# Kernel tuning notes

Hardware: AMD Instinct MI355X
Metric: run time of the kernel (lower is better)

The kernel has to match this reference:

```python
import jax, jax.numpy as jnp
import numpy as np

B, S, D = 2, 2048, 1024
H, KV, HD = 16, 4, 64
E, TOPK, F = 8, 2, 2048
EPS = 1e-5
THETA = 10000.0


def setup_inputs() -> dict:
    key = jax.random.key(0)
    ks = jax.random.split(key, 12)
    sc = 0.02
    x = jax.random.normal(ks[0], (B, S, D), jnp.float32)
    # real RoPE tables
    inv = 1.0 / (THETA ** (np.arange(0, HD, 2, dtype=np.float32) / HD))
    t = np.arange(S, dtype=np.float32)
    f = np.outer(t, inv)  # [S, HD/2]
    freqs_cos = jnp.asarray(np.cos(f), jnp.float32)
    freqs_sin = jnp.asarray(np.sin(f), jnp.float32)
    return {
        "x": x,
        "freqs_cos": freqs_cos,
        "freqs_sin": freqs_sin,
        "attn_norm_w": jnp.ones((D,), jnp.float32),
        "ffn_norm_w": jnp.ones((D,), jnp.float32),
        "wq": jax.random.normal(ks[1], (D, H * HD), jnp.float32) * sc,
        "wk": jax.random.normal(ks[2], (D, KV * HD), jnp.float32) * sc,
        "wv": jax.random.normal(ks[3], (D, KV * HD), jnp.float32) * sc,
        "wo": jax.random.normal(ks[4], (H * HD, D), jnp.float32) * sc,
        "gate_w": jax.random.normal(ks[5], (D, E), jnp.float32) * sc,
        "w1": jax.random.normal(ks[6], (E, D, F), jnp.float32) * sc,
        "w2": jax.random.normal(ks[7], (E, F, D), jnp.float32) * sc,
        "w3": jax.random.normal(ks[8], (E, D, F), jnp.float32) * sc,
    }


def rmsnorm(x, w):
    return x * jax.lax.rsqrt(jnp.mean(x * x, axis=-1, keepdims=True) + EPS) * w


def apply_rope(xq, cos, sin):
    # xq: [B,S,h,HD]; cos/sin: [S, HD/2]
    xr, xi = xq[..., 0::2], xq[..., 1::2]
    c = cos[None, :, None, :]
    s = sin[None, :, None, :]
    out = jnp.stack([xr * c - xi * s, xr * s + xi * c], axis=-1)
    return out.reshape(xq.shape)


def attention(xn, freqs_cos, freqs_sin, wq, wk, wv, wo):
    q = (xn @ wq).reshape(B, S, H, HD)
    k = (xn @ wk).reshape(B, S, KV, HD)
    v = (xn @ wv).reshape(B, S, KV, HD)
    q = apply_rope(q, freqs_cos, freqs_sin)
    k = apply_rope(k, freqs_cos, freqs_sin)
    n_rep = H // KV
    k = jnp.repeat(k, n_rep, axis=2)  # [B,S,H,HD]
    v = jnp.repeat(v, n_rep, axis=2)
    scores = jnp.einsum("bqhd,bkhd->bhqk", q, k) / jnp.sqrt(jnp.float32(HD))
    causal = jnp.tril(jnp.ones((S, S), bool))
    scores = jnp.where(causal[None, None], scores, jnp.finfo(scores.dtype).min)
    probs = jax.nn.softmax(scores, axis=-1)
    out = jnp.einsum("bhqk,bkhd->bqhd", probs, v).reshape(B, S, H * HD)
    return out @ wo


def sparse_moe(hn, gate_w, w1, w2, w3):
    xf = hn.reshape(-1, D)  # [T, D]
    probs = jax.nn.softmax(xf @ gate_w, axis=-1)  # [T, E]
    topv, topi = jax.lax.top_k(probs, TOPK)
    topv = topv / jnp.sum(topv, axis=-1, keepdims=True)
    # dense [T, E] routing weights (0 for non-selected experts)
    wdense = jnp.sum(jax.nn.one_hot(topi, E, dtype=xf.dtype) * topv[..., None], axis=1)
    h1 = jax.nn.silu(jnp.einsum("td,edf->etf", xf, w1))
    h3 = jnp.einsum("td,edf->etf", xf, w3)
    y = jnp.einsum("etf,efd->etd", h1 * h3, w2)
    out = jnp.einsum("te,etd->td", wdense, y)
    return out.reshape(B, S, D)


def reference(x, freqs_cos, freqs_sin, attn_norm_w, ffn_norm_w,
              wq, wk, wv, wo, gate_w, w1, w2, w3):
    h = x + attention(rmsnorm(x, attn_norm_w), freqs_cos, freqs_sin, wq, wk, wv, wo)
    out = h + sparse_moe(rmsnorm(h, ffn_norm_w), gate_w, w1, w2, w3)
    return out
```

## Files before the change

### kernel.cpp

```cpp
#include <hip/hip_runtime.h>
#include <stdint.h>

typedef unsigned short u16;
typedef unsigned int u32;
typedef __attribute__((ext_vector_type(8))) short short8;
typedef __attribute__((ext_vector_type(8))) u16 us8;
typedef __attribute__((ext_vector_type(4))) u16 us4;
typedef __attribute__((ext_vector_type(4))) float f32x4;

constexpr int NB = 2;
constexpr int SEQ = 2048;
constexpr int DIM = 1024;
constexpr int NH = 16;
constexpr int HD = 64;
constexpr int NE = 8;
constexpr int FF = 2048;
constexpr int TOK = NB * SEQ;
constexpr int NQKV = 1536;
constexpr int NPAIR = TOK * 2;
constexpr float REPS = 1e-5f;

#define VMCNT(n) asm volatile("s_waitcnt vmcnt(" #n ")" ::: "memory")
#define LGKM0 asm volatile("s_waitcnt lgkmcnt(0)" ::: "memory")

__device__ __forceinline__ u16 f2bf(float x) {
  union { float f; u32 u; } v; v.f = x;
  u32 r = v.u + 0x7fffu + ((v.u >> 16) & 1u);
  return (u16)(r >> 16);
}
__device__ __forceinline__ float bf2f(u16 h) {
  union { u32 u; float f; } v; v.u = ((u32)h) << 16;
  return v.f;
}

__device__ __forceinline__ void gl_lds16(const u16* g, u16* l) {
  __builtin_amdgcn_global_load_lds(
      (const __attribute__((address_space(1))) void*)g,
      (__attribute__((address_space(3))) void*)l, 16, 0, 0);
}

template <bool SPLIT>
__global__ __launch_bounds__(256) void tcvt_k(const float* __restrict__ src,
                                              u16* __restrict__ dhi,
                                              u16* __restrict__ dlo,
                                              int K, int N) {
  int z = blockIdx.z;
  src += (size_t)z * K * N;
  dhi += (size_t)z * K * N;
  if (SPLIT) dlo += (size_t)z * K * N;
  int n0 = blockIdx.x * 64, k0 = blockIdx.y * 64;
  __shared__ float tile[64][65];
  int t = threadIdx.x;
  int kk = t >> 4, nn4 = (t & 15) * 4;
#pragma unroll
  for (int i = 0; i < 4; i++) {
    int k = kk + i * 16;
    const float* p = src + (size_t)(k0 + k) * N + n0 + nn4;
    float4 v = *(const float4*)p;
    tile[nn4 + 0][k] = v.x;
    tile[nn4 + 1][k] = v.y;
    tile[nn4 + 2][k] = v.z;
    tile[nn4 + 3][k] = v.w;
  }
  __syncthreads();
  int nn = t >> 4, k4 = (t & 15) * 4;
#pragma unroll
  for (int i = 0; i < 4; i++) {
    int n = nn + i * 16;
    us4 hi, lo;
#pragma unroll
    for (int j = 0; j < 4; j++) {
      float f = tile[n][k4 + j];
      u16 h = f2bf(f);
      hi[j] = h;
      if (SPLIT) lo[j] = f2bf(f - bf2f(h));
    }
    *(us4*)(dhi + (size_t)(n0 + n) * K + k0 + k4) = hi;
    if (SPLIT) *(us4*)(dlo + (size_t)(n0 + n) * K + k0 + k4) = lo;
  }
}

template <bool SPLIT>
__global__ __launch_bounds__(256) void rmsnorm_k(const float* __restrict__ x,
                                                 const float* __restrict__ w,
                                                 u16* __restrict__ ohi,
                                                 u16* __restrict__ olo) {
  int row = blockIdx.x, t = threadIdx.x;
  float4 v = *(const float4*)(x + (size_t)row * DIM + t * 4);
  float ss = v.x * v.x + v.y * v.y + v.z * v.z + v.w * v.w;
#pragma unroll
  for (int m = 1; m < 64; m <<= 1) ss += __shfl_xor(ss, m);
  __shared__ float red[4];
  if ((t & 63) == 0) red[t >> 6] = ss;
  __syncthreads();
  float rstd = rsqrtf((red[0] + red[1] + red[2] + red[3]) * (1.0f / DIM) + REPS);
  float4 wv = *(const float4*)(w + t * 4);
  float os[4] = {v.x * rstd * wv.x, v.y * rstd * wv.y, v.z * rstd * wv.z,
                 v.w * rstd * wv.w};
  us4 hi, lo;
#pragma unroll
  for (int j = 0; j < 4; j++) {
    u16 h = f2bf(os[j]);
    hi[j] = h;
    if (SPLIT) lo[j] = f2bf(os[j] - bf2f(h));
  }
  *(us4*)(ohi + (size_t)row * DIM + t * 4) = hi;
  if (SPLIT) *(us4*)(olo + (size_t)row * DIM + t * 4) = lo;
}

template <int EPI, bool SPLIT, bool DUAL, bool PERSIST, int NXL, int NT, int BN>
__global__ __launch_bounds__(256, 2) void gemm_k(
    const u16* __restrict__ Ah, const u16* __restrict__ Al,
    const u16* __restrict__ Bh, const u16* __restrict__ Bl,
    const u16* __restrict__ B1, int N, int ldc,
    float* __restrict__ Cf, u16* __restrict__ Cb, float* __restrict__ C2,
    const float* __restrict__ resid, const int* __restrict__ cnt,
    const int* __restrict__ pids, const float* __restrict__ pw,
    const int* __restrict__ plan) {
  constexpr int K = NT * 32;
  constexpr int WCOL = BN / 2;
  constexpr int FN = WCOL / 16;
  constexpr int NAI = 2;
  constexpr int NBI = BN / 64;
  constexpr int BUFA = 128 * 32;
  constexpr int BUFB = BN * 32;
  constexpr bool L6 = SPLIT || DUAL;

  int tid = threadIdx.x, lane = tid & 63, wid = tid >> 6;
  int wm = wid >> 1, wn = wid & 1;
  int rr = lane & 15, g = lane >> 4;

  __shared__ u16 sAh[3 * BUFA];
  __shared__ u16 sAl[SPLIT ? 3 * BUFA : 16];
  __shared__ u16 sBh[3 * BUFB];
  __shared__ u16 sBl[SPLIT ? 3 * BUFB : 16];
  __shared__ u16 sB1[DUAL ? 3 * BUFB : 16];
  __shared__ int spid[PERSIST ? 128 : 8];
  __shared__ int srow[PERSIST ? 128 : 8];

  int pl[9];
  int items;
  if (PERSIST) {
#pragma unroll
    for (int e = 0; e < 9; e++) pl[e] = plan[e];
    items = pl[8] << NXL;
  } else {
    items = 1;
  }

  int it0 = PERSIST ? blockIdx.x : 0;
  int itstep = PERSIST ? gridDim.x : 1;
  for (int w = it0; w < items; w += itstep) {
    int m0, n0, z, cntz;
    if (PERSIST) {
      int wy = w >> NXL;
      int x = w & ((1 << NXL) - 1);
      z = 0;
#pragma unroll
      for (int e = 1; e < 8; e++) z += (wy >= pl[e]) ? 1 : 0;
      int yt = wy - pl[z];
      m0 = yt * 128;
      n0 = x * BN;
      cntz = cnt[z];
      if (tid < 128) {
        int i = m0 + tid;
        if (i > cntz - 1) i = cntz - 1;
        int p = pids[z * NPAIR + i];
        spid[tid] = p;
        srow[tid] = (EPI == 2) ? (p >> 1) : p;
      }
      __syncthreads();
    } else {
      m0 = blockIdx.y * 128;
      n0 = blockIdx.x * BN;
      z = 0;
      cntz = 1 << 30;
    }

    const u16* Bhz = Bh + (size_t)z * N * K;
    const u16* Blz = SPLIT ? Bl + (size_t)z * N * K : nullptr;
    const u16* B1z = DUAL ? B1 + (size_t)z * N * K : nullptr;

    int p4 = lane & 3;
    const u16 *agh[NAI], *agl[NAI];
    int aoff[NAI];
#pragma unroll
    for (int i = 0; i < NAI; i++) {
      int rl = i * 64 + wid * 16 + (lane >> 2);
      int gr = PERSIST ? srow[rl] : (m0 + rl);
      int sc = p4 ^ ((rl >> 1) & 3);
      agh[i] = Ah + (size_t)gr * K + sc * 8;
      if (SPLIT) agl[i] = Al + (size_t)gr * K + sc * 8;
      aoff[i] = (i * 4 + wid) * 512;
    }
    const u16 *bgh[NBI], *bgl[NBI], *bg1[NBI];
    int boff[NBI];
#pragma unroll
    for (int i = 0; i < NBI; i++) {
      int rl = i * 64 + wid * 16 + (lane >> 2);
      int sc = p4 ^ ((rl >> 1) & 3);
      size_t gr = (size_t)(n0 + rl) * K + sc * 8;
      bgh[i] = Bhz + gr;
      if (SPLIT) bgl[i] = Blz + gr;
      if (DUAL) bg1[i] = B1z + gr;
      boff[i] = (i * 4 + wid) * 512;
    }

    auto STAGE = [&](int kt, int bi) {
      int k0 = kt * 32;
#pragma unroll
      for (int i = 0; i < NAI; i++) {
        gl_lds16(agh[i] + k0, sAh + bi * BUFA + aoff[i]);
        if (SPLIT) gl_lds16(agl[i] + k0, sAl + bi * BUFA + aoff[i]);
      }
#pragma unroll
      for (int i = 0; i < NBI; i++) {
        gl_lds16(bgh[i] + k0, sBh + bi * BUFB + boff[i]);
        if (SPLIT) gl_lds16(bgl[i] + k0, sBl + bi * BUFB + boff[i]);
        if (DUAL) gl_lds16(bg1[i] + k0, sB1 + bi * BUFB + boff[i]);
      }
    };

    f32x4 zv = {0.f, 0.f, 0.f, 0.f};
    f32x4 acc[4][FN];
    f32x4 acc1[DUAL ? 4 : 1][DUAL ? FN : 1];
#pragma unroll
    for (int a = 0; a < 4; a++)
#pragma unroll
      for (int b = 0; b < FN; b++) {
        acc[a][b] = zv;
        if (DUAL) acc1[a][b] = zv;
      }

    STAGE(0, 0);
    STAGE(1, 1);
    STAGE(2, 2);

    int bi = 0;
    for (int t = 0; t < NT; t++) {
      int og = NT - 1 - t;
      if (L6) {
        if (og >= 2) VMCNT(12);
        else if (og == 1) VMCNT(6);
        else VMCNT(0);
      } else {
        if (og >= 2) VMCNT(8);
        else if (og == 1) VMCNT(4);
        else VMCNT(0);
      }
      __builtin_amdgcn_s_barrier();

      const u16* bA = sAh + bi * BUFA;
      const u16* bAl = sAl + (SPLIT ? bi * BUFA : 0);
      const u16* bB = sBh + bi * BUFB;
      const u16* bBl = sBl + (SPLIT ? bi * BUFB : 0);
      const u16* bB1 = sB1 + (DUAL ? bi * BUFB : 0);

      short8 a_h[4], a_l[4], b_h[FN], b_l[FN], b1f[FN];
#pragma unroll
      for (int f = 0; f < 4; f++) {
        int ra = wm * 64 + f * 16 + rr;
        int off = ra * 32 + ((g ^ ((ra >> 1) & 3)) * 8);
        a_h[f] = *(const short8*)&bA[off];
        if (SPLIT) a_l[f] = *(const short8*)&bAl[off];
      }
#pragma unroll
      for (int f = 0; f < FN; f++) {
        int rb = wn * WCOL + f * 16 + rr;
        int off = rb * 32 + ((g ^ ((rb >> 1) & 3)) * 8);
        b_h[f] = *(const short8*)&bB[off];
        if (SPLIT) b_l[f] = *(const short8*)&bBl[off];
        if (DUAL) b1f[f] = *(const short8*)&bB1[off];
      }
#pragma unroll
      for (int fm = 0; fm < 4; fm++)
#pragma unroll
        for (int fn = 0; fn < FN; fn++) {
          acc[fm][fn] = __builtin_amdgcn_mfma_f32_16x16x32_bf16(
              a_h[fm], b_h[fn], acc[fm][fn], 0, 0, 0);
          if (SPLIT) {
            acc[fm][fn] = __builtin_amdgcn_mfma_f32_16x16x32_bf16(
                a_h[fm], b_l[fn], acc[fm][fn], 0, 0, 0);
            acc[fm][fn] = __builtin_amdgcn_mfma_f32_16x16x32_bf16(
                a_l[fm], b_h[fn], acc[fm][fn], 0, 0, 0);
          }
          if (DUAL)
            acc1[fm][fn] = __builtin_amdgcn_mfma_f32_16x16x32_bf16(
                a_h[fm], b1f[fn], acc1[fm][fn], 0, 0, 0);
        }

      LGKM0;
      __builtin_amdgcn_s_barrier();
      if (t + 3 < NT) STAGE(t + 3, bi);
      bi = (bi == 2) ? 0 : bi + 1;
    }

#pragma unroll
    for (int fm = 0; fm < 4; fm++)
#pragma unroll
      for (int fn = 0; fn < FN; fn++)
#pragma unroll
        for (int rg = 0; rg < 4; rg++) {
          int rl = wm * 64 + fm * 16 + g * 4 + rg;
          int col = n0 + wn * WCOL + fn * 16 + rr;
          float v = acc[fm][fn][rg];
          if (EPI == 0) {
            Cf[(size_t)(m0 + rl) * ldc + col] = v;
          } else if (EPI == 1) {
            size_t idx = (size_t)(m0 + rl) * ldc + col;
            float r2 = v + resid[idx];
            Cf[idx] = r2;
            C2[idx] = r2;
          } else if (EPI == 2) {
            if (m0 + rl < cntz) {
              float gg = v / (1.0f + __expf(-v));
              float o = gg * acc1[fm][fn][rg];
              Cb[(size_t)spid[rl] * ldc + col] = f2bf(o);
            }
          } else {
            if (m0 + rl < cntz) {
              int p = spid[rl];
              atomicAdd(&Cf[(size_t)(p >> 1) * ldc + col], pw[p] * v);
            }
          }
        }
    if (PERSIST) __syncthreads();
  }
}

__global__ __launch_bounds__(256) void rope_k(float* __restrict__ qkv,
                                              const float* __restrict__ fc,
                                              const float* __restrict__ fs) {
  int idx = blockIdx.x * 256 + threadIdx.x;
  int i = idx & 31;
  int hh = (idx >> 5) % 20;
  int t = idx / 640;
  if (t >= TOK) return;
  int s = t & (SEQ - 1);
  int base = (hh < 16) ? (hh * 64) : (1024 + (hh - 16) * 64);
  float c = fc[s * 32 + i], sn = fs[s * 32 + i];
  float* p = qkv + (size_t)t * NQKV + base + 2 * i;
  float xr = p[0], xi = p[1];
  p[0] = xr * c - xi * sn;
  p[1] = xr * sn + xi * c;
}

__global__ __launch_bounds__(256) void cvtkv_k(const float* __restrict__ qkv,
                                               u16* __restrict__ Kh,
                                               u16* __restrict__ Kl,
                                               u16* __restrict__ Vh,
                                               u16* __restrict__ Vl) {
  int kvt = blockIdx.x;
  int kvh = blockIdx.y;
  int b = blockIdx.z;
  int t = threadIdx.x;
  __shared__ float vt[64][65];
  size_t tile = ((size_t)((b * 4 + kvh) * 32 + kvt)) * 4096;
  int r = t >> 2, c4 = t & 3;
  {
    const float* kp = qkv + ((size_t)(b * SEQ + kvt * 64 + r)) * NQKV + 1024 +
                      kvh * 64 + c4 * 16;
    float ff[16];
#pragma unroll
    for (int q = 0; q < 4; q++) {
      float4 f = *(const float4*)(kp + q * 4);
      ff[q * 4 + 0] = f.x; ff[q * 4 + 1] = f.y;
      ff[q * 4 + 2] = f.z; ff[q * 4 + 3] = f.w;
    }
#pragma unroll
    for (int half = 0; half < 2; half++) {
      int c = c4 * 2 + half;
      us8 hi, lo;
#pragma unroll
      for (int j = 0; j < 8; j++) {
        float f = ff[half * 8 + j];
        u16 h = f2bf(f);
        hi[j] = h;
        lo[j] = f2bf(f - bf2f(h));
      }
      int off = r * 64 + ((c ^ (r & 7)) * 8);
      *(us8*)(Kh + tile + off) = hi;
      *(us8*)(Kl + tile + off) = lo;
    }
  }
  {
    const float* vp = qkv + ((size_t)(b * SEQ + kvt * 64 + r)) * NQKV + 1280 +
                      kvh * 64 + c4 * 16;
#pragma unroll
    for (int q = 0; q < 4; q++) {
      float4 f = *(const float4*)(vp + q * 4);
      vt[r][c4 * 16 + q * 4 + 0] = f.x;
      vt[r][c4 * 16 + q * 4 + 1] = f.y;
      vt[r][c4 * 16 + q * 4 + 2] = f.z;
      vt[r][c4 * 16 + q * 4 + 3] = f.w;
    }
  }
  __syncthreads();
  {
    int d = t >> 2, g4 = t & 3;
    float ff[16];
#pragma unroll
    for (int j = 0; j < 16; j++) ff[j] = vt[g4 * 16 + j][d];
#pragma unroll
    for (int half = 0; half < 2; half++) {
      int c = g4 * 2 + half;
      us8 hi, lo;
#pragma unroll
      for (int j = 0; j < 8; j++) {
        float f = ff[half * 8 + j];
        u16 h = f2bf(f);
        hi[j] = h;
        lo[j] = f2bf(f - bf2f(h));
      }
      int off = d * 64 + ((c ^ (d & 7)) * 8);
      *(us8*)(Vh + tile + off) = hi;
      *(us8*)(Vl + tile + off) = lo;
    }
  }
}

__global__ __launch_bounds__(256, 2) void flash_k(
    const float* __restrict__ qkv, const u16* __restrict__ Kg,
    const u16* __restrict__ Klg, const u16* __restrict__ Vg,
    const u16* __restrict__ Vlg, u16* __restrict__ ah, u16* __restrict__ al) {
  int pi = blockIdx.x;
  int h = blockIdx.y;
  int b = blockIdx.z;
  int qt[2] = {31 - pi, pi};
  int kvh = h >> 2;
  int tid = threadIdx.x, lane = tid & 63, wid = tid >> 6;
  int rr = lane & 15, g = lane >> 4;

  __shared__ u16 sKh[4096], sKl[4096], sVh[4096], sVl[4096];
  __shared__ u32 sP[4][1024];

  f32x4 zv = {0.f, 0.f, 0.f, 0.f};
  short8 aqh[2][2], aql[2][2];
#pragma unroll
  for (int u = 0; u < 2; u++) {
    int qrow = qt[u] * 64 + wid * 16 + rr;
    const float* qp =
        qkv + ((size_t)(b * SEQ + qrow)) * NQKV + h * 64 + g * 8;
#pragma unroll
    for (int kc = 0; kc < 2; kc++) {
      float4 f0 = *(const float4*)(qp + kc * 32);
      float4 f1 = *(const float4*)(qp + kc * 32 + 4);
      float ff[8] = {f0.x, f0.y, f0.z, f0.w, f1.x, f1.y, f1.z, f1.w};
#pragma unroll
      for (int j = 0; j < 8; j++) {
        u16 hi = f2bf(ff[j]);
        aqh[u][kc][j] = (short)hi;
        aql[u][kc][j] = (short)f2bf(ff[j] - bf2f(hi));
      }
    }
  }

  f32x4 o[2][4];
  float m_r[2][4], l_r[2][4];
#pragma unroll
  for (int u = 0; u < 2; u++)
#pragma unroll
    for (int i = 0; i < 4; i++) {
      o[u][i] = zv;
      m_r[u][i] = -3.0e38f;
      l_r[u][i] = 0.f;
    }

  size_t tb = ((size_t)(b * 4 + kvh) * 32) * 4096;
  int so = tid * 16;
  us8 rKh[2], rKl[2], rVh[2], rVl[2];
  {
    size_t go = tb + so;
    rKh[0] = *(const us8*)(Kg + go);  rKh[1] = *(const us8*)(Kg + go + 8);
    rKl[0] = *(const us8*)(Klg + go); rKl[1] = *(const us8*)(Klg + go + 8);
    rVh[0] = *(const us8*)(Vg + go);  rVh[1] = *(const us8*)(Vg + go + 8);
    rVl[0] = *(const us8*)(Vlg + go); rVl[1] = *(const us8*)(Vlg + go + 8);
  }

  int nt = qt[0];
  for (int kvt = 0; kvt <= nt; kvt++) {
    __syncthreads();
    *(us8*)&sKh[so] = rKh[0]; *(us8*)&sKh[so + 8] = rKh[1];
    *(us8*)&sKl[so] = rKl[0]; *(us8*)&sKl[so + 8] = rKl[1];
    *(us8*)&sVh[so] = rVh[0]; *(us8*)&sVh[so + 8] = rVh[1];
    *(us8*)&sVl[so] = rVl[0]; *(us8*)&sVl[so + 8] = rVl[1];
    if (kvt < nt) {
      size_t go = tb + (size_t)(kvt + 1) * 4096 + so;
      rKh[0] = *(const us8*)(Kg + go);  rKh[1] = *(const us8*)(Kg + go + 8);
      rKl[0] = *(const us8*)(Klg + go); rKl[1] = *(const us8*)(Klg + go + 8);
      rVh[0] = *(const us8*)(Vg + go);  rVh[1] = *(const us8*)(Vg + go + 8);
      rVl[0] = *(const us8*)(Vlg + go); rVl[1] = *(const us8*)(Vlg + go + 8);
    }
    __syncthreads();

#pragma unroll
    for (int u = 0; u < 2; u++) {
      if (!(u == 1 && kvt > qt[1])) {
        float pv[4][4];
#pragma unroll
        for (int c16 = 0; c16 < 4; c16++) {
          int rk = c16 * 16 + rr;
          f32x4 sacc = zv;
#pragma unroll
          for (int kc = 0; kc < 2; kc++) {
            int sw = rk * 64 + (((kc * 4 + g) ^ (rk & 7)) * 8);
            short8 bh = *(const short8*)&sKh[sw];
            short8 bl = *(const short8*)&sKl[sw];
            sacc = __builtin_amdgcn_mfma_f32_16x16x32_bf16(aqh[u][kc], bh,
                                                           sacc, 0, 0, 0);
            sacc = __builtin_amdgcn_mfma_f32_16x16x32_bf16(aqh[u][kc], bl,
                                                           sacc, 0, 0, 0);
            sacc = __builtin_amdgcn_mfma_f32_16x16x32_bf16(aql[u][kc], bh,
                                                           sacc, 0, 0, 0);
          }
          bool diag = (kvt == qt[u]);
#pragma unroll
          for (int rg = 0; rg < 4; rg++) {
            float val = sacc[rg] * 0.125f;
            if (diag) {
              int kv_l = c16 * 16 + rr;
              int q_l = wid * 16 + g * 4 + rg;
              if (kv_l > q_l) val = -3.0e38f;
            }
            pv[c16][rg] = val;
          }
        }
        float pm[4];
#pragma unroll
        for (int rg = 0; rg < 4; rg++)
          pm[rg] = fmaxf(fmaxf(pv[0][rg], pv[1][rg]),
                         fmaxf(pv[2][rg], pv[3][rg]));
#pragma unroll
        for (int m = 1; m < 16; m <<= 1)
#pragma unroll
          for (int rg = 0; rg < 4; rg++)
            pm[rg] = fmaxf(pm[rg], __shfl_xor(pm[rg], m));
        float scl[4];
#pragma unroll
        for (int rg = 0; rg < 4; rg++) {
          float mn = fmaxf(m_r[u][rg], pm[rg]);
          scl[rg] = __expf(m_r[u][rg] - mn);
          m_r[u][rg] = mn;
        }
#pragma unroll
        for (int c16 = 0; c16 < 4; c16++)
#pragma unroll
          for (int rg = 0; rg < 4; rg++)
            pv[c16][rg] = __expf(pv[c16][rg] - m_r[u][rg]);
        float rsum[4];
#pragma unroll
        for (int rg = 0; rg < 4; rg++)
          rsum[rg] = pv[0][rg] + pv[1][rg] + pv[2][rg] + pv[3][rg];
#pragma unroll
        for (int m = 1; m < 16; m <<= 1)
#pragma unroll
          for (int rg = 0; rg < 4; rg++) rsum[rg] += __shfl_xor(rsum[rg], m);
#pragma unroll
        for (int rg = 0; rg < 4; rg++)
          l_r[u][rg] = l_r[u][rg] * scl[rg] + rsum[rg];
#pragma unroll
        for (int d16 = 0; d16 < 4; d16++)
#pragma unroll
          for (int rg = 0; rg < 4; rg++) o[u][d16][rg] *= scl[rg];

#pragma unroll
        for (int c16 = 0; c16 < 4; c16++)
#pragma unroll
          for (int rg = 0; rg < 4; rg++) {
            int ql = g * 4 + rg;
            int kvl = c16 * 16 + rr;
            u16 hi = f2bf(pv[c16][rg]);
            u16 lo = f2bf(pv[c16][rg] - bf2f(hi));
            sP[wid][ql * 64 + (kvl ^ (((ql >> 2) & 3) << 4))] =
                ((u32)lo << 16) | (u32)hi;
          }
        short8 pah[2], pal[2];
#pragma unroll
        for (int kc = 0; kc < 2; kc++) {
          int xb = (kc * 32 + g * 8) ^ (((rr >> 2) & 3) << 4);
          const u32* pp = &sP[wid][rr * 64 + xb];
#pragma unroll
          for (int j = 0; j < 8; j++) {
            u32 w = pp[j];
            pah[kc][j] = (short)(w & 0xffffu);
            pal[kc][j] = (short)(w >> 16);
          }
        }
#pragma unroll
        for (int d16 = 0; d16 < 4; d16++) {
          int rv = d16 * 16 + rr;
#pragma unroll
          for (int kc = 0; kc < 2; kc++) {
            int sw = rv * 64 + (((kc * 4 + g) ^ (rv & 7)) * 8);
            short8 vh = *(const short8*)&sVh[sw];
            short8 vl = *(const short8*)&sVl[sw];
            o[u][d16] = __builtin_amdgcn_mfma_f32_16x16x32_bf16(
                pah[kc], vh, o[u][d16], 0, 0, 0);
            o[u][d16] = __builtin_amdgcn_mfma_f32_16x16x32_bf16(
                pah[kc], vl, o[u][d16], 0, 0, 0);
            o[u][d16] = __builtin_amdgcn_mfma_f32_16x16x32_bf16(
                pal[kc], vh, o[u][d16], 0, 0, 0);
          }
        }
      }
    }
  }

#pragma unroll
  for (int u = 0; u < 2; u++)
#pragma unroll
    for (int rg = 0; rg < 4; rg++) {
      float inv = 1.0f / l_r[u][rg];
      int qr = qt[u] * 64 + wid * 16 + g * 4 + rg;
      size_t obase = (size_t)(b * SEQ + qr) * 1024 + h * 64;
#pragma unroll
      for (int d16 = 0; d16 < 4; d16++) {
        float v = o[u][d16][rg] * inv;
        u16 hi = f2bf(v);
        ah[obase + d16 * 16 + rr] = hi;
        al[obase + d16 * 16 + rr] = f2bf(v - bf2f(hi));
      }
    }
}

__global__ __launch_bounds__(256) void route_k(const float* __restrict__ h,
                                               const float* __restrict__ wffn,
                                               const float* __restrict__ gw,
                                               int* __restrict__ cnt,
                                               int* __restrict__ pids,
                                               float* __restrict__ pw) {
  int t = blockIdx.x, tid = threadIdx.x;
  float4 v = *(const float4*)(h + (size_t)t * DIM + tid * 4);
  float ss = v.x * v.x + v.y * v.y + v.z * v.z + v.w * v.w;
#pragma unroll
  for (int m = 1; m < 64; m <<= 1) ss += __shfl_xor(ss, m);
  __shared__ float red[4];
  if ((tid & 63) == 0) red[tid >> 6] = ss;
  __syncthreads();
  float rstd = rsqrtf((red[0] + red[1] + red[2] + red[3]) * (1.0f / DIM) + REPS);
  float4 wv = *(const float4*)(wffn + tid * 4);
  float xn[4] = {v.x * rstd * wv.x, v.y * rstd * wv.y, v.z * rstd * wv.z,
                 v.w * rstd * wv.w};
  float pl[8] = {0, 0, 0, 0, 0, 0, 0, 0};
#pragma unroll
  for (int j = 0; j < 4; j++) {
    const float* gp = gw + (size_t)(tid * 4 + j) * 8;
    float4 g0 = *(const float4*)gp;
    float4 g1 = *(const float4*)(gp + 4);
    pl[0] += xn[j] * g0.x; pl[1] += xn[j] * g0.y;
    pl[2] += xn[j] * g0.z; pl[3] += xn[j] * g0.w;
    pl[4] += xn[j] * g1.x; pl[5] += xn[j] * g1.y;
    pl[6] += xn[j] * g1.z; pl[7] += xn[j] * g1.w;
  }
#pragma unroll
  for (int e = 0; e < 8; e++)
#pragma unroll
    for (int m = 1; m < 64; m <<= 1) pl[e] += __shfl_xor(pl[e], m);
  __shared__ float lred[4][8];
  if ((tid & 63) == 0)
#pragma unroll
    for (int e = 0; e < 8; e++) lred[tid >> 6][e] = pl[e];
  __syncthreads();
  if (tid == 0) {
    float lg[8];
#pragma unroll
    for (int e = 0; e < 8; e++)
      lg[e] = lred[0][e] + lred[1][e] + lred[2][e] + lred[3][e];
    int e1 = 0;
    float l1 = lg[0];
#pragma unroll
    for (int e = 1; e < 8; e++)
      if (lg[e] > l1) { l1 = lg[e]; e1 = e; }
    int e2 = -1;
    float l2 = -3.0e38f;
#pragma unroll
    for (int e = 0; e < 8; e++)
      if (e != e1 && lg[e] > l2) { l2 = lg[e]; e2 = e; }
    float w1 = 1.0f / (1.0f + expf(l2 - l1));
    float w2 = 1.0f / (1.0f + expf(l1 - l2));
    int p0 = atomicAdd(&cnt[e1], 1);
    pids[e1 * NPAIR + p0] = t * 2;
    pw[t * 2] = w1;
    int p1 = atomicAdd(&cnt[e2], 1);
    pids[e2 * NPAIR + p1] = t * 2 + 1;
    pw[t * 2 + 1] = w2;
  }
}

__global__ void zero_k(int* cnt) {
  if (threadIdx.x < 8) cnt[threadIdx.x] = 0;
}

__global__ void plan_k(const int* __restrict__ cnt, int* __restrict__ plan) {
  if (threadIdx.x == 0) {
    int acc = 0;
    for (int e = 0; e < 8; e++) {
      plan[e] = acc;
      acc += (cnt[e] + 127) >> 7;
    }
    plan[8] = acc;
  }
}

extern "C" void kernel_launch(void* const* d_in, const int* in_sizes, int n_in,
                              void* d_out, int out_size, void* d_ws,
                              size_t ws_size, hipStream_t stream) {
  (void)in_sizes; (void)n_in; (void)out_size; (void)ws_size;
  const float* x = (const float*)d_in[0];
  const float* fc = (const float*)d_in[1];
  const float* fs = (const float*)d_in[2];
  const float* anw = (const float*)d_in[3];
  const float* fnw = (const float*)d_in[4];
  const float* wq = (const float*)d_in[5];
  const float* wk = (const float*)d_in[6];
  const float* wv = (const float*)d_in[7];
  const float* wo = (const float*)d_in[8];
  const float* gw = (const float*)d_in[9];
  const float* w1 = (const float*)d_in[10];
  const float* w2 = (const float*)d_in[11];
  const float* w3 = (const float*)d_in[12];
  float* outf = (float*)d_out;

  char* ws = (char*)d_ws;
  size_t off = 0;
  auto alloc = [&](size_t bytes) {
    void* p = ws + off;
    off += (bytes + 255) & ~(size_t)255;
    return p;
  };
  u16* wqkvT_h = (u16*)alloc((size_t)NQKV * DIM * 2);
  u16* wqkvT_l = (u16*)alloc((size_t)NQKV * DIM * 2);
  u16* woT_h = (u16*)alloc((size_t)DIM * DIM * 2);
  u16* woT_l = (u16*)alloc((size_t)DIM * DIM * 2);
  u16* w1T = (u16*)alloc((size_t)NE * FF * DIM * 2);
  u16* w3T = (u16*)alloc((size_t)NE * FF * DIM * 2);
  u16* w2T = (u16*)alloc((size_t)NE * DIM * FF * 2);
  u16* xnh = (u16*)alloc((size_t)TOK * DIM * 2);
  u16* xnl = (u16*)alloc((size_t)TOK * DIM * 2);
  float* qkvf = (float*)alloc((size_t)TOK * NQKV * 4);
  u16* attnh = (u16*)alloc((size_t)TOK * DIM * 2);
  u16* attnl = (u16*)alloc((size_t)TOK * DIM * 2);
  float* hbuf = (float*)alloc((size_t)TOK * DIM * 4);
  u16* hn = (u16*)alloc((size_t)TOK * DIM * 2);
  u16* h13 = (u16*)alloc((size_t)NPAIR * FF * 2);
  int* cnt = (int*)alloc(64);
  int* plan = (int*)alloc(64);
  int* pids = (int*)alloc((size_t)NE * NPAIR * 4);
  float* pwbuf = (float*)alloc((size_t)NPAIR * 4);
  u16* Ksw_h = (u16*)alloc((size_t)NB * 4 * SEQ * 64 * 2);
  u16* Ksw_l = (u16*)alloc((size_t)NB * 4 * SEQ * 64 * 2);
  u16* Vsw_h = (u16*)alloc((size_t)NB * 4 * SEQ * 64 * 2);
  u16* Vsw_l = (u16*)alloc((size_t)NB * 4 * SEQ * 64 * 2);

  dim3 blk(256);
  hipLaunchKernelGGL((tcvt_k<true>), dim3(16, 16, 1), blk, 0, stream, wq,
                     wqkvT_h, wqkvT_l, 1024, 1024);
  hipLaunchKernelGGL((tcvt_k<true>), dim3(4, 16, 1), blk, 0, stream, wk,
                     wqkvT_h + 1024 * 1024, wqkvT_l + 1024 * 1024, 1024, 256);
  hipLaunchKernelGGL((tcvt_k<true>), dim3(4, 16, 1), blk, 0, stream, wv,
                     wqkvT_h + 1280 * 1024, wqkvT_l + 1280 * 1024, 1024, 256);
  hipLaunchKernelGGL((tcvt_k<true>), dim3(16, 16, 1), blk, 0, stream, wo, woT_h,
                     woT_l, 1024, 1024);
  hipLaunchKernelGGL((tcvt_k<false>), dim3(32, 16, 8), blk, 0, stream, w1, w1T,
                     (u16*)nullptr, 1024, 2048);
  hipLaunchKernelGGL((tcvt_k<false>), dim3(32, 16, 8), blk, 0, stream, w3, w3T,
                     (u16*)nullptr, 1024, 2048);
  hipLaunchKernelGGL((tcvt_k<false>), dim3(16, 32, 8), blk, 0, stream, w2, w2T,
                     (u16*)nullptr, 2048, 1024);
  hipLaunchKernelGGL((rmsnorm_k<true>), dim3(TOK), blk, 0, stream, x, anw, xnh,
                     xnl);
  hipLaunchKernelGGL((gemm_k<0, true, false, false, 0, 32, 64>),
                     dim3(NQKV / 64, TOK / 128, 1), blk, 0, stream, xnh, xnl,
                     wqkvT_h, wqkvT_l, (const u16*)nullptr, NQKV, NQKV, qkvf,
                     (u16*)nullptr, (float*)nullptr, (const float*)nullptr,
                     (const int*)nullptr, (const int*)nullptr,
                     (const float*)nullptr, (const int*)nullptr);
  hipLaunchKernelGGL(rope_k, dim3((TOK * 20 * 32) / 256), blk, 0, stream, qkvf,
                     fc, fs);
  hipLaunchKernelGGL(cvtkv_k, dim3(SEQ / 64, 4, NB), blk, 0, stream, qkvf,
                     Ksw_h, Ksw_l, Vsw_h, Vsw_l);
  hipLaunchKernelGGL(flash_k, dim3(16, NH, NB), blk, 0, stream, qkvf, Ksw_h,
                     Ksw_l, Vsw_h, Vsw_l, attnh, attnl);
  hipLaunchKernelGGL((gemm_k<1, true, false, false, 0, 32, 64>),
                     dim3(DIM / 64, TOK / 128, 1), blk, 0, stream, attnh, attnl,
                     woT_h, woT_l, (const u16*)nullptr, DIM, DIM, hbuf,
                     (u16*)nullptr, outf, x, (const int*)nullptr,
                     (const int*)nullptr, (const float*)nullptr,
                     (const int*)nullptr);
  hipLaunchKernelGGL((rmsnorm_k<false>), dim3(TOK), blk, 0, stream, hbuf, fnw,
                     hn, (u16*)nullptr);
  hipLaunchKernelGGL(zero_k, dim3(1), dim3(64), 0, stream, cnt);
  hipLaunchKernelGGL(route_k, dim3(TOK), blk, 0, stream, hbuf, fnw, gw, cnt,
                     pids, pwbuf);
  hipLaunchKernelGGL(plan_k, dim3(1), dim3(64), 0, stream, cnt, plan);
  hipLaunchKernelGGL((gemm_k<2, false, true, true, 4, 32, 128>), dim3(1024),
                     blk, 0, stream, hn, (const u16*)nullptr, w1T,
                     (const u16*)nullptr, w3T, FF, FF, (float*)nullptr, h13,
                     (float*)nullptr, (const float*)nullptr, cnt, pids, pwbuf,
                     plan);
  hipLaunchKernelGGL((gemm_k<3, false, false, true, 3, 64, 128>), dim3(1024),
                     blk, 0, stream, h13, (const u16*)nullptr, w2T,
                     (const u16*)nullptr, (const u16*)nullptr, DIM, DIM, outf,
                     (u16*)nullptr, (float*)nullptr, (const float*)nullptr, cnt,
                     pids, pwbuf, plan);
}
```

Before: 617.0 us.

## Replace triple-buffered GEMM pipeline with single-buffer BK=64 tiles and compact MoE rows

```diff
diff --git a/kernel.cpp b/kernel.cpp
--- a/kernel.cpp
+++ b/kernel.cpp
@@ -19,9 +19,6 @@
 constexpr int NQKV = 1536;
 constexpr int NPAIR = TOK * 2;
 constexpr float REPS = 1e-5f;
-
-#define VMCNT(n) asm volatile("s_waitcnt vmcnt(" #n ")" ::: "memory")
-#define LGKM0 asm volatile("s_waitcnt lgkmcnt(0)" ::: "memory")
 
 __device__ __forceinline__ u16 f2bf(float x) {
   union { float f; u32 u; } v; v.f = x;
@@ -108,35 +105,31 @@
   if (SPLIT) *(us4*)(olo + (size_t)row * DIM + t * 4) = lo;
 }
 
-template <int EPI, bool SPLIT, bool DUAL, bool PERSIST, int NXL, int NT, int BN>
+template <int EPI, bool SPLIT, bool DUAL, bool PERSIST, bool GATHER, int NXL,
+          int NT, int BN>
 __global__ __launch_bounds__(256, 2) void gemm_k(
     const u16* __restrict__ Ah, const u16* __restrict__ Al,
     const u16* __restrict__ Bh, const u16* __restrict__ Bl,
-    const u16* __restrict__ B1, int N, int ldc,
+    const u16* __restrict__ Bd, int N, int ldc,
     float* __restrict__ Cf, u16* __restrict__ Cb, float* __restrict__ C2,
     const float* __restrict__ resid, const int* __restrict__ cnt,
     const int* __restrict__ pids, const float* __restrict__ pw,
     const int* __restrict__ plan) {
-  constexpr int K = NT * 32;
+  constexpr int K = NT * 64;
   constexpr int WCOL = BN / 2;
-  constexpr int FN = WCOL / 16;
-  constexpr int NAI = 2;
-  constexpr int NBI = BN / 64;
-  constexpr int BUFA = 128 * 32;
-  constexpr int BUFB = BN * 32;
-  constexpr bool L6 = SPLIT || DUAL;
+  constexpr int FN = BN / 32;
 
   int tid = threadIdx.x, lane = tid & 63, wid = tid >> 6;
   int wm = wid >> 1, wn = wid & 1;
   int rr = lane & 15, g = lane >> 4;
 
-  __shared__ u16 sAh[3 * BUFA];
-  __shared__ u16 sAl[SPLIT ? 3 * BUFA : 16];
-  __shared__ u16 sBh[3 * BUFB];
-  __shared__ u16 sBl[SPLIT ? 3 * BUFB : 16];
-  __shared__ u16 sB1[DUAL ? 3 * BUFB : 16];
+  __shared__ u16 sAh[128 * 64];
+  __shared__ u16 sAl[SPLIT ? 128 * 64 : 16];
+  __shared__ u16 sBh[BN * 64];
+  __shared__ u16 sBl[SPLIT ? BN * 64 : 16];
+  __shared__ u16 sB1[DUAL ? BN * 64 : 16];
   __shared__ int spid[PERSIST ? 128 : 8];
-  __shared__ int srow[PERSIST ? 128 : 8];
+  __shared__ int srow[GATHER ? 128 : 8];
 
   int pl[9];
   int items;
@@ -151,75 +144,63 @@
   int it0 = PERSIST ? blockIdx.x : 0;
   int itstep = PERSIST ? gridDim.x : 1;
   for (int w = it0; w < items; w += itstep) {
-    int m0, n0, z, cntz;
+    int m0, n0, z, yt, cntz;
     if (PERSIST) {
       int wy = w >> NXL;
       int x = w & ((1 << NXL) - 1);
       z = 0;
 #pragma unroll
       for (int e = 1; e < 8; e++) z += (wy >= pl[e]) ? 1 : 0;
-      int yt = wy - pl[z];
-      m0 = yt * 128;
+      yt = wy - pl[z];
+      m0 = wy * 128;
       n0 = x * BN;
       cntz = cnt[z];
+      __syncthreads();
       if (tid < 128) {
-        int i = m0 + tid;
+        int i = yt * 128 + tid;
         if (i > cntz - 1) i = cntz - 1;
         int p = pids[z * NPAIR + i];
         spid[tid] = p;
-        srow[tid] = (EPI == 2) ? (p >> 1) : p;
+        if (GATHER) srow[tid] = p >> 1;
       }
       __syncthreads();
     } else {
       m0 = blockIdx.y * 128;
       n0 = blockIdx.x * BN;
       z = 0;
+      yt = 0;
       cntz = 1 << 30;
     }
 
     const u16* Bhz = Bh + (size_t)z * N * K;
     const u16* Blz = SPLIT ? Bl + (size_t)z * N * K : nullptr;
-    const u16* B1z = DUAL ? B1 + (size_t)z * N * K : nullptr;
-
-    int p4 = lane & 3;
-    const u16 *agh[NAI], *agl[NAI];
-    int aoff[NAI];
-#pragma unroll
-    for (int i = 0; i < NAI; i++) {
-      int rl = i * 64 + wid * 16 + (lane >> 2);
-      int gr = PERSIST ? srow[rl] : (m0 + rl);
-      int sc = p4 ^ ((rl >> 1) & 3);
+    const u16* Bdz = DUAL ? Bd + (size_t)z * N * K : nullptr;
+
+    const u16 *agh[4], *agl[SPLIT ? 4 : 1];
+    int aoff[4];
+#pragma unroll
+    for (int i = 0; i < 4; i++) {
+      int cid = tid + i * 256;
+      int r = cid >> 3, c = cid & 7;
+      int gr = GATHER ? srow[r] : (m0 + r);
+      int sc = c ^ (r & 7);
       agh[i] = Ah + (size_t)gr * K + sc * 8;
       if (SPLIT) agl[i] = Al + (size_t)gr * K + sc * 8;
-      aoff[i] = (i * 4 + wid) * 512;
-    }
-    const u16 *bgh[NBI], *bgl[NBI], *bg1[NBI];
-    int boff[NBI];
-#pragma unroll
-    for (int i = 0; i < NBI; i++) {
-      int rl = i * 64 + wid * 16 + (lane >> 2);
-      int sc = p4 ^ ((rl >> 1) & 3);
-      size_t gr = (size_t)(n0 + rl) * K + sc * 8;
+      aoff[i] = r * 64 + c * 8;
+    }
+    const u16 *bgh[FN], *bgl[SPLIT ? FN : 1], *bg1[DUAL ? FN : 1];
+    int boff[FN];
+#pragma unroll
+    for (int i = 0; i < FN; i++) {
+      int cid = tid + i * 256;
+      int r = cid >> 3, c = cid & 7;
+      int sc = c ^ (r & 7);
+      size_t gr = (size_t)(n0 + r) * K + sc * 8;
       bgh[i] = Bhz + gr;
       if (SPLIT) bgl[i] = Blz + gr;
-      if (DUAL) bg1[i] = B1z + gr;
-      boff[i] = (i * 4 + wid) * 512;
-    }
-
-    auto STAGE = [&](int kt, int bi) {
-      int k0 = kt * 32;
-#pragma unroll
-      for (int i = 0; i < NAI; i++) {
-        gl_lds16(agh[i] + k0, sAh + bi * BUFA + aoff[i]);
-        if (SPLIT) gl_lds16(agl[i] + k0, sAl + bi * BUFA + aoff[i]);
-      }
-#pragma unroll
-      for (int i = 0; i < NBI; i++) {
-        gl_lds16(bgh[i] + k0, sBh + bi * BUFB + boff[i]);
-        if (SPLIT) gl_lds16(bgl[i] + k0, sBl + bi * BUFB + boff[i]);
-        if (DUAL) gl_lds16(bg1[i] + k0, sB1 + bi * BUFB + boff[i]);
-      }
-    };
+      if (DUAL) bg1[i] = Bdz + gr;
+      boff[i] = r * 64 + c * 8;
+    }
 
     f32x4 zv = {0.f, 0.f, 0.f, 0.f};
     f32x4 acc[4][FN];
@@ -232,67 +213,58 @@
         if (DUAL) acc1[a][b] = zv;
       }
 
-    STAGE(0, 0);
-    STAGE(1, 1);
-    STAGE(2, 2);
-
-    int bi = 0;
     for (int t = 0; t < NT; t++) {
-      int og = NT - 1 - t;
-      if (L6) {
-        if (og >= 2) VMCNT(12);
-        else if (og == 1) VMCNT(6);
-        else VMCNT(0);
-      } else {
-        if (og >= 2) VMCNT(8);
-        else if (og == 1) VMCNT(4);
-        else VMCNT(0);
-      }
-      __builtin_amdgcn_s_barrier();
-
-      const u16* bA = sAh + bi * BUFA;
-      const u16* bAl = sAl + (SPLIT ? bi * BUFA : 0);
-      const u16* bB = sBh + bi * BUFB;
-      const u16* bBl = sBl + (SPLIT ? bi * BUFB : 0);
-      const u16* bB1 = sB1 + (DUAL ? bi * BUFB : 0);
-
-      short8 a_h[4], a_l[4], b_h[FN], b_l[FN], b1f[FN];
-#pragma unroll
-      for (int f = 0; f < 4; f++) {
-        int ra = wm * 64 + f * 16 + rr;
-        int off = ra * 32 + ((g ^ ((ra >> 1) & 3)) * 8);
-        a_h[f] = *(const short8*)&bA[off];
-        if (SPLIT) a_l[f] = *(const short8*)&bAl[off];
-      }
-#pragma unroll
-      for (int f = 0; f < FN; f++) {
-        int rb = wn * WCOL + f * 16 + rr;
-        int off = rb * 32 + ((g ^ ((rb >> 1) & 3)) * 8);
-        b_h[f] = *(const short8*)&bB[off];
-        if (SPLIT) b_l[f] = *(const short8*)&bBl[off];
-        if (DUAL) b1f[f] = *(const short8*)&bB1[off];
-      }
-#pragma unroll
-      for (int fm = 0; fm < 4; fm++)
-#pragma unroll
-        for (int fn = 0; fn < FN; fn++) {
-          acc[fm][fn] = __builtin_amdgcn_mfma_f32_16x16x32_bf16(
-              a_h[fm], b_h[fn], acc[fm][fn], 0, 0, 0);
-          if (SPLIT) {
+      int k0 = t * 64;
+      __syncthreads();
+#pragma unroll
+      for (int i = 0; i < 4; i++) {
+        gl_lds16(agh[i] + k0, sAh + aoff[i]);
+        if (SPLIT) gl_lds16(agl[i] + k0, sAl + aoff[i]);
+      }
+#pragma unroll
+      for (int i = 0; i < FN; i++) {
+        gl_lds16(bgh[i] + k0, sBh + boff[i]);
+        if (SPLIT) gl_lds16(bgl[i] + k0, sBl + boff[i]);
+        if (DUAL) gl_lds16(bg1[i] + k0, sB1 + boff[i]);
+      }
+      __syncthreads();
+
+#pragma unroll
+      for (int kc = 0; kc < 2; kc++) {
+        short8 a_h[4], a_l[SPLIT ? 4 : 1], b_h[FN], b_l[SPLIT ? FN : 1],
+            b1f[DUAL ? FN : 1];
+#pragma unroll
+        for (int f = 0; f < 4; f++) {
+          int ra = wm * 64 + f * 16 + rr;
+          int off = ra * 64 + (((kc * 4 + g) ^ (ra & 7)) * 8);
+          a_h[f] = *(const short8*)&sAh[off];
+          if (SPLIT) a_l[f] = *(const short8*)&sAl[off];
+        }
+#pragma unroll
+        for (int f = 0; f < FN; f++) {
+          int rb = wn * WCOL + f * 16 + rr;
+          int off = rb * 64 + (((kc * 4 + g) ^ (rb & 7)) * 8);
+          b_h[f] = *(const short8*)&sBh[off];
+          if (SPLIT) b_l[f] = *(const short8*)&sBl[off];
+          if (DUAL) b1f[f] = *(const short8*)&sB1[off];
+        }
+#pragma unroll
+        for (int fm = 0; fm < 4; fm++)
+#pragma unroll
+          for (int fn = 0; fn < FN; fn++) {
             acc[fm][fn] = __builtin_amdgcn_mfma_f32_16x16x32_bf16(
-                a_h[fm], b_l[fn], acc[fm][fn], 0, 0, 0);
-            acc[fm][fn] = __builtin_amdgcn_mfma_f32_16x16x32_bf16(
-                a_l[fm], b_h[fn], acc[fm][fn], 0, 0, 0);
+                a_h[fm], b_h[fn], acc[fm][fn], 0, 0, 0);
+            if (SPLIT) {
+              acc[fm][fn] = __builtin_amdgcn_mfma_f32_16x16x32_bf16(
+                  a_h[fm], b_l[fn], acc[fm][fn], 0, 0, 0);
+              acc[fm][fn] = __builtin_amdgcn_mfma_f32_16x16x32_bf16(
+                  a_l[fm], b_h[fn], acc[fm][fn], 0, 0, 0);
+            }
+            if (DUAL)
+              acc1[fm][fn] = __builtin_amdgcn_mfma_f32_16x16x32_bf16(
+                  a_h[fm], b1f[fn], acc1[fm][fn], 0, 0, 0);
           }
-          if (DUAL)
-            acc1[fm][fn] = __builtin_amdgcn_mfma_f32_16x16x32_bf16(
-                a_h[fm], b1f[fn], acc1[fm][fn], 0, 0, 0);
-        }
-
-      LGKM0;
-      __builtin_amdgcn_s_barrier();
-      if (t + 3 < NT) STAGE(t + 3, bi);
-      bi = (bi == 2) ? 0 : bi + 1;
+      }
     }
 
 #pragma unroll
@@ -312,19 +284,17 @@
             Cf[idx] = r2;
             C2[idx] = r2;
           } else if (EPI == 2) {
-            if (m0 + rl < cntz) {
-              float gg = v / (1.0f + __expf(-v));
-              float o = gg * acc1[fm][fn][rg];
-              Cb[(size_t)spid[rl] * ldc + col] = f2bf(o);
-            }
+            float gg = v / (1.0f + __expf(-v));
+            float o = gg * acc1[fm][fn][rg];
+            Cb[(size_t)(m0 + rl) * ldc + col] = f2bf(o);
           } else {
-            if (m0 + rl < cntz) {
+            int i = yt * 128 + rl;
+            if (i < cntz) {
               int p = spid[rl];
               atomicAdd(&Cf[(size_t)(p >> 1) * ldc + col], pw[p] * v);
             }
           }
         }
-    if (PERSIST) __syncthreads();
   }
 }
 
@@ -728,6 +698,10 @@
     off += (bytes + 255) & ~(size_t)255;
     return p;
   };
+  u16* xnh = (u16*)alloc((size_t)TOK * DIM * 2);
+  u16* xnl = (u16*)alloc((size_t)TOK * DIM * 2);
+  float* qkvf = (float*)alloc((size_t)TOK * NQKV * 4);
+  u16* h13 = xnh;
   u16* wqkvT_h = (u16*)alloc((size_t)NQKV * DIM * 2);
   u16* wqkvT_l = (u16*)alloc((size_t)NQKV * DIM * 2);
   u16* woT_h = (u16*)alloc((size_t)DIM * DIM * 2);
@@ -735,14 +709,10 @@
   u16* w1T = (u16*)alloc((size_t)NE * FF * DIM * 2);
   u16* w3T = (u16*)alloc((size_t)NE * FF * DIM * 2);
   u16* w2T = (u16*)alloc((size_t)NE * DIM * FF * 2);
-  u16* xnh = (u16*)alloc((size_t)TOK * DIM * 2);
-  u16* xnl = (u16*)alloc((size_t)TOK * DIM * 2);
-  float* qkvf = (float*)alloc((size_t)TOK * NQKV * 4);
   u16* attnh = (u16*)alloc((size_t)TOK * DIM * 2);
   u16* attnl = (u16*)alloc((size_t)TOK * DIM * 2);
   float* hbuf = (float*)alloc((size_t)TOK * DIM * 4);
   u16* hn = (u16*)alloc((size_t)TOK * DIM * 2);
-  u16* h13 = (u16*)alloc((size_t)NPAIR * FF * 2);
   int* cnt = (int*)alloc(64);
   int* plan = (int*)alloc(64);
   int* pids = (int*)alloc((size_t)NE * NPAIR * 4);
@@ -769,7 +739,7 @@
                      (u16*)nullptr, 2048, 1024);
   hipLaunchKernelGGL((rmsnorm_k<true>), dim3(TOK), blk, 0, stream, x, anw, xnh,
                      xnl);
-  hipLaunchKernelGGL((gemm_k<0, true, false, false, 0, 32, 64>),
+  hipLaunchKernelGGL((gemm_k<0, true, false, false, false, 0, 16, 64>),
                      dim3(NQKV / 64, TOK / 128, 1), blk, 0, stream, xnh, xnl,
                      wqkvT_h, wqkvT_l, (const u16*)nullptr, NQKV, NQKV, qkvf,
                      (u16*)nullptr, (float*)nullptr, (const float*)nullptr,
@@ -781,7 +751,7 @@
                      Ksw_h, Ksw_l, Vsw_h, Vsw_l);
   hipLaunchKernelGGL(flash_k, dim3(16, NH, NB), blk, 0, stream, qkvf, Ksw_h,
                      Ksw_l, Vsw_h, Vsw_l, attnh, attnl);
-  hipLaunchKernelGGL((gemm_k<1, true, false, false, 0, 32, 64>),
+  hipLaunchKernelGGL((gemm_k<1, true, false, false, false, 0, 16, 64>),
                      dim3(DIM / 64, TOK / 128, 1), blk, 0, stream, attnh, attnl,
                      woT_h, woT_l, (const u16*)nullptr, DIM, DIM, hbuf,
                      (u16*)nullptr, outf, x, (const int*)nullptr,
@@ -793,13 +763,13 @@
   hipLaunchKernelGGL(route_k, dim3(TOK), blk, 0, stream, hbuf, fnw, gw, cnt,
                      pids, pwbuf);
   hipLaunchKernelGGL(plan_k, dim3(1), dim3(64), 0, stream, cnt, plan);
-  hipLaunchKernelGGL((gemm_k<2, false, true, true, 4, 32, 128>), dim3(1024),
-                     blk, 0, stream, hn, (const u16*)nullptr, w1T,
+  hipLaunchKernelGGL((gemm_k<2, false, true, true, true, 4, 16, 128>),
+                     dim3(512), blk, 0, stream, hn, (const u16*)nullptr, w1T,
                      (const u16*)nullptr, w3T, FF, FF, (float*)nullptr, h13,
                      (float*)nullptr, (const float*)nullptr, cnt, pids, pwbuf,
                      plan);
-  hipLaunchKernelGGL((gemm_k<3, false, false, true, 3, 64, 128>), dim3(1024),
-                     blk, 0, stream, h13, (const u16*)nullptr, w2T,
+  hipLaunchKernelGGL((gemm_k<3, false, false, true, false, 3, 32, 128>),
+                     dim3(512), blk, 0, stream, h13, (const u16*)nullptr, w2T,
                      (const u16*)nullptr, (const u16*)nullptr, DIM, DIM, outf,
                      (u16*)nullptr, (float*)nullptr, (const float*)nullptr, cnt,
                      pids, pwbuf, plan);
```

Measured after the change: 579.8 us. 6.0% less time.
